# Kernel tuning notes

Hardware: AMD Instinct MI355X
Metric: run time of the kernel (lower is better)

The kernel has to match this reference:

```python
import math
import jax, jax.numpy as jnp
import numpy as np

# irreps_in == irreps_out == 256x0e + 256x1o + 128x2e
# (start, end, mul, ir_dim) for each irrep block in the flat feature vector
SEGS = [(0, 256, 256, 1), (256, 1024, 256, 3), (1024, 1664, 128, 5)]
DIM = 1664
BATCH = 32768
NW = sum(m * m for _, _, m, _ in SEGS)  # 147456
NB = 256  # bias only on scalar (0e) output


def setup_inputs() -> dict:
    key = jax.random.key(0)
    k1, k2, k3 = jax.random.split(key, 3)
    ws = jax.random.normal(k1, (NW,), dtype=jnp.float32)
    bs = jax.random.normal(k2, (NB,), dtype=jnp.float32)
    x = jax.random.normal(k3, (BATCH, DIM), dtype=jnp.float32)
    return {"ws": ws, "bs": bs, "x": x}


def reference(ws, bs, x):
    # Block-diagonal equivariant linear. Each instruction:
    #   out[i_out] += einsum('uw,ui->wi', w, x_block) / sqrt(mul_in * fan_in)
    # Here in/out irreps match 1:1, so fan_in = 1 for every output.
    w_off = 0
    outs = []
    for (s, e, mul, d) in SEGS:
        w = ws[w_off:w_off + mul * mul].reshape(mul, mul)
        w_off += mul * mul
        xb = x[:, s:e].reshape(-1, mul, d)  # [B, u, i]
        o = jnp.einsum('uw,bui->bwi', w, xb) * (1.0 / math.sqrt(mul))
        outs.append(o.reshape(-1, mul * d))
    # bias on the scalar (0e) output block only
    outs[0] = outs[0] + bs
    return jnp.concatenate(outs, axis=-1)  # [B, 1664]
```

## Files before the change

### kernel.cpp

```cpp
#include <hip/hip_runtime.h>


typedef short short8 __attribute__((ext_vector_type(8)));
typedef float f32x4 __attribute__((ext_vector_type(4)));

#define DIMF 1664

__device__ __forceinline__ unsigned short f2bf(float f) {
  unsigned int u = __float_as_uint(f);
  u += 0x7fffu + ((u >> 16) & 1u);
  return (unsigned short)(u >> 16);
}

__device__ __forceinline__ void gload16(const float* g, float* l) {
  __builtin_amdgcn_global_load_lds(
      (const __attribute__((address_space(1))) void*)g,
      (__attribute__((address_space(3))) void*)l, 16, 0, 0);
}

__global__ __launch_bounds__(256) void prep_w(const float* __restrict__ ws,
                                              unsigned short* __restrict__ wf) {
  int t = blockIdx.x * blockDim.x + threadIdx.x;
  int MUL, woff, goff;
  float scale;
  if (t < 8192) {
    MUL = 256; woff = 0; goff = 0; scale = 0.0625f;
  } else if (t < 16384) {
    MUL = 256; woff = 65536; goff = 8192; scale = 0.0625f;
  } else if (t < 18432) {
    MUL = 128; woff = 131072; goff = 16384; scale = 0.088388347648318447f;
  } else {
    return;
  }
  int g = t - goff;
  int l = g & 63;
  int nks = MUL >> 5;
  int ks = (g >> 6) % nks;
  int nt = g / (64 * nks);
  int n = nt * 16 + (l & 15);
  int kb = ks * 32 + (l >> 4) * 8;
  short8 v;
#pragma unroll
  for (int j = 0; j < 8; ++j)
    v[j] = (short)f2bf(ws[woff + (size_t)(kb + j) * MUL + n] * scale);
  *reinterpret_cast<short8*>(wf + (size_t)t * 8) = v;
}

template <int MUL, int D, int BMB, int GR, int GSF, bool BIAS>
__device__ __forceinline__ void seg_run(const float* __restrict__ x,
                                        const unsigned short* __restrict__ wf,
                                        const float* __restrict__ bs,
                                        float* __restrict__ out, int blk, int s,
                                        float* A32) {
  constexpr int SEGW = MUL * D;
  constexpr int ISS = GR * SEGW / 256;
  constexpr int NGRP = BMB / GR;
  constexpr int NISS = NGRP * ISS;
  constexpr int MT = BMB * D;
  constexpr int NMT = MT / 16;
  constexpr int NTW = MUL / 64;
  constexpr int NKS = MUL / 32;

  const int tid = threadIdx.x;
  const int lane = tid & 63;
  const int wave = tid >> 6;
  const int l15 = lane & 15;
  const int lhi = lane >> 4;
  const int b0 = blk * BMB;

  for (int m = wave; m < NISS; m += 4) {
    int g = m / ISS;
    int j = m - g * ISS;
    int q = j * 256 + lane * 4;
    int r = g * GR + q / SEGW;
    int c = q % SEGW;
    gload16(x + (size_t)(b0 + r) * DIMF + s + c, A32 + g * GSF + j * 256);
  }
  asm volatile("s_waitcnt vmcnt(0)" ::: "memory");
  __syncthreads();

  int rowoff[NMT];
#pragma unroll
  for (int mt = 0; mt < NMT; ++mt) {
    int ar = mt * 16 + l15;
    int b = ar / D;
    int i = ar - b * D;
    rowoff[mt] = (b / GR) * GSF + (b % GR) * SEGW + i;
  }

  f32x4 acc[NMT][NTW];
#pragma unroll
  for (int a = 0; a < NMT; ++a)
#pragma unroll
    for (int b = 0; b < NTW; ++b) acc[a][b] = (f32x4){0.f, 0.f, 0.f, 0.f};

#pragma unroll
  for (int ks = 0; ks < NKS; ++ks) {
    short8 af[NMT];
#pragma unroll
    for (int mt = 0; mt < NMT; ++mt) {
      if (D == 1) {
        f32x4 lo = *reinterpret_cast<const f32x4*>(&A32[rowoff[mt] + ks * 32 + lhi * 8]);
        f32x4 hi =
            *reinterpret_cast<const f32x4*>(&A32[rowoff[mt] + ks * 32 + lhi * 8 + 4]);
#pragma unroll
        for (int j = 0; j < 4; ++j) {
          af[mt][j] = (short)f2bf(lo[j]);
          af[mt][j + 4] = (short)f2bf(hi[j]);
        }
      } else {
#pragma unroll
        for (int j = 0; j < 8; ++j)
          af[mt][j] = (short)f2bf(A32[rowoff[mt] + (ks * 32 + lhi * 8 + j) * D]);
      }
    }
#pragma unroll
    for (int nt = 0; nt < NTW; ++nt) {
      int ntg = wave * NTW + nt;
      short8 bfr = *reinterpret_cast<const short8*>(
          wf + ((size_t)(ntg * NKS + ks) * 64 + lane) * 8);
#pragma unroll
      for (int mt = 0; mt < NMT; ++mt)
        acc[mt][nt] =
            __builtin_amdgcn_mfma_f32_16x16x32_bf16(af[mt], bfr, acc[mt][nt], 0, 0, 0);
    }
  }

#pragma unroll
  for (int nt = 0; nt < NTW; ++nt) {
    int n = wave * (MUL / 4) + nt * 16 + l15;
    float bias = 0.f;
    if (BIAS) bias = bs[n];
#pragma unroll
    for (int mt = 0; mt < NMT; ++mt) {
#pragma unroll
      for (int q = 0; q < 4; ++q) {
        int m = mt * 16 + lhi * 4 + q;
        int b = m / D;
        int i = m - b * D;
        out[(size_t)(b0 + b) * DIMF + s + n * D + i] = acc[mt][nt][q] + bias;
      }
    }
  }
}

__global__ __launch_bounds__(256) void linear_main(const float* __restrict__ x,
                                                   const unsigned short* __restrict__ wf,
                                                   const float* __restrict__ bs,
                                                   float* __restrict__ out) {
  __shared__ __align__(16) float A32[12352];
  int blk = blockIdx.x;
  if (blk < 1024) {
    seg_run<256, 1, 32, 1, 260, true>(x, wf, bs, out, blk, 0, A32);
  } else if (blk < 3072) {
    seg_run<256, 3, 16, 1, 772, false>(x, wf + 65536, bs, out, blk - 1024, 256, A32);
  } else {
    seg_run<128, 5, 16, 2, 1288, false>(x, wf + 131072, bs, out, blk - 3072, 1024, A32);
  }
}

extern "C" void kernel_launch(void* const* d_in, const int* in_sizes, int n_in,
                              void* d_out, int out_size, void* d_ws, size_t ws_size,
                              hipStream_t stream) {
  const float* ws = (const float*)d_in[0];
  const float* bs = (const float*)d_in[1];
  const float* x = (const float*)d_in[2];
  float* out = (float*)d_out;
  unsigned short* wf = (unsigned short*)d_ws;

  hipLaunchKernelGGL(prep_w, dim3(72), dim3(256), 0, stream, ws, wf);
  hipLaunchKernelGGL(linear_main, dim3(1024 + 2048 + 2048), dim3(256), 0, stream, x,
                     wf, bs, out);
}
```

Before: 127.8 us.

## Pipeline x loads with double-buffered K-chunks and persistent tiles per block

Each block now processes several batch tiles (TPB=8), splitting K into chunks that are double-buffered in LDS. The global-to-LDS DMA for the next chunk is issued before computing on the current one, so load latency overlaps with MFMA work. For the d>1 segments, an explicit de-interleave pass converts the fp32 strided layout into a padded bf16 [row][u] layout, which replaces strided scalar LDS reads with vector short8 loads. The grid shrinks from 5120 to 768 blocks and LDS use grows, which lowers occupancy and adds extra barriers per step.

```diff
diff --git a/kernel.cpp b/kernel.cpp
--- a/kernel.cpp
+++ b/kernel.cpp
@@ -17,6 +17,16 @@
       (const __attribute__((address_space(1))) void*)g,
       (__attribute__((address_space(3))) void*)l, 16, 0, 0);
 }
+
+__device__ __forceinline__ void barrier_c() {
+  asm volatile("s_waitcnt lgkmcnt(0)" ::: "memory");
+  __builtin_amdgcn_s_barrier();
+  asm volatile("" ::: "memory");
+}
+
+#define WAITVM(N) asm volatile("s_waitcnt vmcnt(%0)" ::: "memory");
+#undef WAITVM
+#define WAITVM(N) asm volatile("s_waitcnt vmcnt(%0)" :: "i"(N) : "memory")
 
 __global__ __launch_bounds__(256) void prep_w(const float* __restrict__ ws,
                                               unsigned short* __restrict__ wf) {
@@ -46,101 +56,155 @@
   *reinterpret_cast<short8*>(wf + (size_t)t * 8) = v;
 }
 
-template <int MUL, int D, int BMB, int GR, int GSF, bool BIAS>
+template <int MUL, int D, int BMB, int KC, int GR, int GSF, int TPB, int S, bool BIAS>
 __device__ __forceinline__ void seg_run(const float* __restrict__ x,
                                         const unsigned short* __restrict__ wf,
                                         const float* __restrict__ bs,
-                                        float* __restrict__ out, int blk, int s,
-                                        float* A32) {
-  constexpr int SEGW = MUL * D;
-  constexpr int ISS = GR * SEGW / 256;
+                                        float* __restrict__ out, int blk, char* lds) {
+  constexpr int CHW = KC * D;
+  constexpr int ISSG = GR * CHW / 256;
   constexpr int NGRP = BMB / GR;
-  constexpr int NISS = NGRP * ISS;
+  constexpr int NISS = NGRP * ISSG;
+  constexpr int KW = NISS / 4;
+  constexpr int NCH = MUL / KC;
+  constexpr int LSZ = NGRP * GSF;
+  constexpr int LDAD = KC + 8;
   constexpr int MT = BMB * D;
   constexpr int NMT = MT / 16;
   constexpr int NTW = MUL / 64;
+  constexpr int NKSC = KC / 32;
   constexpr int NKS = MUL / 32;
+  constexpr int NQ4 = NISS / 4;
+  constexpr int STEPS = TPB * NCH;
+
+  float* L0 = (float*)lds;
+  unsigned short* Dd = (unsigned short*)(lds + 2 * LSZ * 4);
 
   const int tid = threadIdx.x;
   const int lane = tid & 63;
   const int wave = tid >> 6;
   const int l15 = lane & 15;
   const int lhi = lane >> 4;
-  const int b0 = blk * BMB;
-
-  for (int m = wave; m < NISS; m += 4) {
-    int g = m / ISS;
-    int j = m - g * ISS;
-    int q = j * 256 + lane * 4;
-    int r = g * GR + q / SEGW;
-    int c = q % SEGW;
-    gload16(x + (size_t)(b0 + r) * DIMF + s + c, A32 + g * GSF + j * 256);
-  }
-  asm volatile("s_waitcnt vmcnt(0)" ::: "memory");
-  __syncthreads();
-
-  int rowoff[NMT];
-#pragma unroll
-  for (int mt = 0; mt < NMT; ++mt) {
-    int ar = mt * 16 + l15;
-    int b = ar / D;
-    int i = ar - b * D;
-    rowoff[mt] = (b / GR) * GSF + (b % GR) * SEGW + i;
-  }
+
+  float bias[NTW];
+  if (BIAS) {
+#pragma unroll
+    for (int nt = 0; nt < NTW; ++nt) bias[nt] = bs[wave * (MUL / 4) + nt * 16 + l15];
+  }
+
+  auto dma = [&](int st) {
+    int tile = st / NCH, ch = st % NCH;
+    int b0 = (blk * TPB + tile) * BMB;
+    float* Lb = L0 + (st & 1) * LSZ;
+#pragma unroll
+    for (int m = wave; m < NISS; m += 4) {
+      int g2 = m / ISSG, j = m - g2 * ISSG;
+      int qg = j * 256 + lane * 4;
+      int rl = qg / CHW;
+      int c = qg - rl * CHW;
+      gload16(x + (size_t)(b0 + g2 * GR + rl) * DIMF + S + ch * CHW + c,
+              Lb + g2 * GSF + j * 256);
+    }
+  };
+
+  auto deint = [&](int st) {
+    const float* Lb = L0 + (st & 1) * LSZ;
+#pragma unroll
+    for (int it = 0; it < NQ4; ++it) {
+      int q4 = tid + it * 256;
+      int m = q4 >> 6, l = q4 & 63;
+      int g2 = m / ISSG, j = m - g2 * ISSG;
+      f32x4 v = *reinterpret_cast<const f32x4*>(Lb + g2 * GSF + j * 256 + l * 4);
+      int qg = j * 256 + l * 4;
+      int rl = qg / CHW;
+      int c = qg - rl * CHW;
+      int u = c / D;
+      int i = c - u * D;
+      int rowb = (g2 * GR + rl) * D;
+#pragma unroll
+      for (int jj = 0; jj < 4; ++jj) {
+        int ii = i + jj;
+        int u2 = u;
+        if (ii >= D) { ii -= D; ++u2; }
+        Dd[(rowb + ii) * LDAD + u2] = f2bf(v[jj]);
+      }
+    }
+  };
 
   f32x4 acc[NMT][NTW];
-#pragma unroll
-  for (int a = 0; a < NMT; ++a)
-#pragma unroll
-    for (int b = 0; b < NTW; ++b) acc[a][b] = (f32x4){0.f, 0.f, 0.f, 0.f};
-
-#pragma unroll
-  for (int ks = 0; ks < NKS; ++ks) {
-    short8 af[NMT];
-#pragma unroll
-    for (int mt = 0; mt < NMT; ++mt) {
-      if (D == 1) {
-        f32x4 lo = *reinterpret_cast<const f32x4*>(&A32[rowoff[mt] + ks * 32 + lhi * 8]);
-        f32x4 hi =
-            *reinterpret_cast<const f32x4*>(&A32[rowoff[mt] + ks * 32 + lhi * 8 + 4]);
-#pragma unroll
-        for (int j = 0; j < 4; ++j) {
-          af[mt][j] = (short)f2bf(lo[j]);
-          af[mt][j + 4] = (short)f2bf(hi[j]);
+
+  dma(0);
+#pragma unroll 1
+  for (int st = 0; st < STEPS; ++st) {
+    const int ch = st % NCH;
+    const int tile = st / NCH;
+    if (st + 1 < STEPS) {
+      dma(st + 1);
+      WAITVM(KW);
+    } else {
+      WAITVM(0);
+    }
+    barrier_c();
+    if (D > 1) {
+      deint(st);
+      barrier_c();
+    }
+    if (ch == 0) {
+#pragma unroll
+      for (int a = 0; a < NMT; ++a)
+#pragma unroll
+        for (int b = 0; b < NTW; ++b) acc[a][b] = (f32x4){0.f, 0.f, 0.f, 0.f};
+    }
+    const float* Lb = L0 + (st & 1) * LSZ;
+#pragma unroll
+    for (int ks = 0; ks < NKSC; ++ks) {
+      short8 af[NMT];
+#pragma unroll
+      for (int mt = 0; mt < NMT; ++mt) {
+        if (D == 1) {
+          const float* p = Lb + (mt * 16 + l15) * GSF + ks * 32 + lhi * 8;
+          f32x4 lo = *reinterpret_cast<const f32x4*>(p);
+          f32x4 hi = *reinterpret_cast<const f32x4*>(p + 4);
+#pragma unroll
+          for (int j = 0; j < 4; ++j) {
+            af[mt][j] = (short)f2bf(lo[j]);
+            af[mt][j + 4] = (short)f2bf(hi[j]);
+          }
+        } else {
+          af[mt] = *reinterpret_cast<const short8*>(
+              &Dd[(mt * 16 + l15) * LDAD + ks * 32 + lhi * 8]);
         }
-      } else {
-#pragma unroll
-        for (int j = 0; j < 8; ++j)
-          af[mt][j] = (short)f2bf(A32[rowoff[mt] + (ks * 32 + lhi * 8 + j) * D]);
-      }
-    }
-#pragma unroll
-    for (int nt = 0; nt < NTW; ++nt) {
-      int ntg = wave * NTW + nt;
-      short8 bfr = *reinterpret_cast<const short8*>(
-          wf + ((size_t)(ntg * NKS + ks) * 64 + lane) * 8);
-#pragma unroll
-      for (int mt = 0; mt < NMT; ++mt)
-        acc[mt][nt] =
-            __builtin_amdgcn_mfma_f32_16x16x32_bf16(af[mt], bfr, acc[mt][nt], 0, 0, 0);
-    }
-  }
-
-#pragma unroll
-  for (int nt = 0; nt < NTW; ++nt) {
-    int n = wave * (MUL / 4) + nt * 16 + l15;
-    float bias = 0.f;
-    if (BIAS) bias = bs[n];
-#pragma unroll
-    for (int mt = 0; mt < NMT; ++mt) {
-#pragma unroll
-      for (int q = 0; q < 4; ++q) {
-        int m = mt * 16 + lhi * 4 + q;
-        int b = m / D;
-        int i = m - b * D;
-        out[(size_t)(b0 + b) * DIMF + s + n * D + i] = acc[mt][nt][q] + bias;
-      }
-    }
+      }
+      int ksg = ch * NKSC + ks;
+#pragma unroll
+      for (int nt = 0; nt < NTW; ++nt) {
+        int ntg = wave * NTW + nt;
+        short8 bfr = *reinterpret_cast<const short8*>(
+            wf + ((size_t)(ntg * NKS + ksg) * 64 + lane) * 8);
+#pragma unroll
+        for (int mt = 0; mt < NMT; ++mt)
+          acc[mt][nt] = __builtin_amdgcn_mfma_f32_16x16x32_bf16(af[mt], bfr,
+                                                                acc[mt][nt], 0, 0, 0);
+      }
+    }
+    if (ch == NCH - 1) {
+      int b0 = (blk * TPB + tile) * BMB;
+#pragma unroll
+      for (int nt = 0; nt < NTW; ++nt) {
+        int n = wave * (MUL / 4) + nt * 16 + l15;
+        float bi = BIAS ? bias[nt] : 0.f;
+#pragma unroll
+        for (int mt = 0; mt < NMT; ++mt)
+#pragma unroll
+          for (int q = 0; q < 4; ++q) {
+            int mm = mt * 16 + lhi * 4 + q;
+            int b = mm / D;
+            int i = mm - b * D;
+            out[(size_t)(b0 + b) * DIMF + S + n * D + i] = acc[mt][nt][q] + bi;
+          }
+      }
+    }
+    if (D == 1) barrier_c();
   }
 }
 
@@ -148,14 +212,16 @@
                                                    const unsigned short* __restrict__ wf,
                                                    const float* __restrict__ bs,
                                                    float* __restrict__ out) {
-  __shared__ __align__(16) float A32[12352];
+  __shared__ __align__(16) char lds[62720];
   int blk = blockIdx.x;
-  if (blk < 1024) {
-    seg_run<256, 1, 32, 1, 260, true>(x, wf, bs, out, blk, 0, A32);
-  } else if (blk < 3072) {
-    seg_run<256, 3, 16, 1, 772, false>(x, wf + 65536, bs, out, blk - 1024, 256, A32);
+  if (blk < 256) {
+    seg_run<256, 1, 16, 256, 1, 260, 8, 0, true>(x, wf, bs, out, blk, lds);
+  } else if (blk < 512) {
+    seg_run<256, 3, 16, 128, 2, 776, 8, 256, false>(x, wf + 65536, bs, out, blk - 256,
+                                                    lds);
   } else {
-    seg_run<128, 5, 16, 2, 1288, false>(x, wf + 131072, bs, out, blk - 3072, 1024, A32);
+    seg_run<128, 5, 16, 64, 4, 1284, 8, 1024, false>(x, wf + 131072, bs, out,
+                                                     blk - 512, lds);
   }
 }
 
@@ -169,6 +235,5 @@
   unsigned short* wf = (unsigned short*)d_ws;
 
   hipLaunchKernelGGL(prep_w, dim3(72), dim3(256), 0, stream, ws, wf);
-  hipLaunchKernelGGL(linear_main, dim3(1024 + 2048 + 2048), dim3(256), 0, stream, x,
-                     wf, bs, out);
-}
+  hipLaunchKernelGGL(linear_main, dim3(768), dim3(256), 0, stream, x, wf, bs, out);
+}
```

After: 158.4 us. 24.0% more time.
